# Performance work log

Measured on AMD Instinct MI355X. Metric: run time of the kernel, lower is better.

Reference implementation:

```python
import jax, jax.numpy as jnp
import numpy as np

E = 128          # embedding_dim
H = 128          # decoder_hidden_dim
N = 200000       # number of candidate nodes


def setup_inputs() -> dict:
    key = jax.random.key(0)
    k0, k1, k2, k3, k4, k5 = jax.random.split(key, 6)
    return {
        "current_node_emb": jax.random.normal(k0, (1, E), jnp.float32),
        "context_emb": jax.random.normal(k1, (1, E), jnp.float32),
        "candidate_node_embs": jax.random.normal(k2, (N, E), jnp.float32),
        "Wq": jax.random.normal(k3, (H, 2 * E), jnp.float32) * 0.05,  # nn.Linear(2E->H, bias=False) weight
        "Wk": jax.random.normal(k4, (H, E), jnp.float32) * 0.05,      # nn.Linear(E->H, bias=False) weight
        "mask": jax.random.randint(k5, (1, N), 0, 2, jnp.int32),
    }


def reference(current_node_emb, context_emb, candidate_node_embs, Wq, Wk, mask):
    # combined_input = cat([current, context], dim=1) -> [1, 2E]
    combined = jnp.concatenate([current_node_emb, context_emb], axis=1)
    query = combined @ Wq.T                      # [1, H]
    keys = candidate_node_embs @ Wk.T            # [N, H]
    attn_scores = query @ keys.T                 # [1, N]
    masked = jnp.where(mask == 0, -jnp.inf, attn_scores)
    probs = jax.nn.softmax(masked, axis=1)       # [1, N]

    n = probs.shape[1]
    k = min(50, max(1, int(0.5 * n)))            # static Python int -> jit-friendly
    top_probs, _ = jax.lax.top_k(probs, k)       # [1, k]
    threshold = top_probs[:, -1:]                # [1, 1]
    top_mask = probs >= threshold
    filtered = probs * top_mask
    filtered = filtered / (jnp.sum(filtered, axis=1, keepdims=True) + 1e-10)

    log_probs_all = jnp.log(filtered + 1e-10)    # [1, N]
    # Categorical(filtered): true-zero probability outside top-k
    logits = jnp.where(filtered > 0, jnp.log(filtered), -jnp.inf)
    action_idx = jax.random.categorical(jax.random.key(42), logits, axis=1)  # [1]
    log_prob_action = jnp.take_along_axis(logits, action_idx[:, None], axis=1)[:, 0]  # [1]
    return (log_probs_all, log_prob_action, action_idx)
```

## Files before the change

### kernel.cpp

```cpp
#include <hip/hip_runtime.h>
#include <math.h>


#define CAP 4096
#define NEG_INF (-__builtin_inff())

__device__ __forceinline__ unsigned int f2ord(float f){
  unsigned int b = __float_as_uint(f);
  return (b & 0x80000000u) ? ~b : (b | 0x80000000u);
}
__device__ __forceinline__ unsigned int rotl32(unsigned int x, int d){
  return (x << d) | (x >> (32 - d));
}

__device__ float gumbel_from_idx(unsigned int idx){
  unsigned int x0 = 0u, x1 = idx;
  const unsigned int ks0 = 0u, ks1 = 42u;
  const unsigned int ks2 = 0u ^ 42u ^ 0x1BD11BDAu;
  x0 += ks0; x1 += ks1;
#define TF_RND(r) { x0 += x1; x1 = rotl32(x1, (r)); x1 ^= x0; }
  TF_RND(13) TF_RND(15) TF_RND(26) TF_RND(6)
  x0 += ks1; x1 += ks2 + 1u;
  TF_RND(17) TF_RND(29) TF_RND(16) TF_RND(24)
  x0 += ks2; x1 += ks0 + 2u;
  TF_RND(13) TF_RND(15) TF_RND(26) TF_RND(6)
  x0 += ks0; x1 += ks1 + 3u;
  TF_RND(17) TF_RND(29) TF_RND(16) TF_RND(24)
  x0 += ks1; x1 += ks2 + 4u;
  TF_RND(13) TF_RND(15) TF_RND(26) TF_RND(6)
  x0 += ks2; x1 += ks0 + 5u;
#undef TF_RND
  unsigned int bits = x0 ^ x1;
  unsigned int fb = (bits >> 9) | 0x3f800000u;
  float f = __uint_as_float(fb) - 1.0f;
  float u = (f < 1.17549435e-38f) ? 1.17549435e-38f : f;
  return -logf(-logf(u));
}

__global__ void k_prep(const float* __restrict__ cur, const float* __restrict__ ctx,
                       const float* __restrict__ Wq, const float* __restrict__ Wk,
                       float* __restrict__ v, unsigned int* __restrict__ hist,
                       unsigned int* __restrict__ scal_u){
  __shared__ float comb[256];
  __shared__ float q[128];
  int t = threadIdx.x;
  for (int k = t; k < 2048; k += 256) hist[k] = 0u;
  if (t < 16) scal_u[t] = 0u;
  comb[t] = (t < 128) ? cur[t] : ctx[t - 128];
  __syncthreads();
  if (t < 128){
    float acc = 0.f;
    const float* row = Wq + t * 256;
    for (int j = 0; j < 256; ++j) acc = fmaf(row[j], comb[j], acc);
    q[t] = acc;
  }
  __syncthreads();
  if (t < 128){
    float acc = 0.f;
    for (int h = 0; h < 128; ++h) acc = fmaf(q[h], Wk[h * 128 + t], acc);
    v[t] = acc;
  }
}

__global__ __launch_bounds__(256) void k_score(const float* __restrict__ cand,
    const int* __restrict__ mask, const float* __restrict__ v,
    float* __restrict__ scores, float* __restrict__ out, int N){
  const float NLOG = logf(1e-10f);
  int t = threadIdx.x;
  int lane = t & 63, wave = t >> 6;
  int hi = lane >> 5, hl = lane & 31;
  float4 v4 = ((const float4*)v)[hl];
  const float4* cp = (const float4*)cand;
  int base = (blockIdx.x * 4 + wave) * 32;
  float4 c[16];
  #pragma unroll
  for (int k = 0; k < 16; ++k){
    int r = base + 2 * k + hi;
    r = (r < N) ? r : (N - 1);
    c[k] = cp[(size_t)r * 32 + hl];
  }
  float p[16];
  #pragma unroll
  for (int k = 0; k < 16; ++k)
    p[k] = fmaf(c[k].x, v4.x, fmaf(c[k].y, v4.y, fmaf(c[k].z, v4.z, c[k].w * v4.w)));
  #pragma unroll
  for (int k = 0; k < 16; ++k){
    p[k] += __shfl_xor(p[k], 1, 64);
    p[k] += __shfl_xor(p[k], 2, 64);
    p[k] += __shfl_xor(p[k], 4, 64);
    p[k] += __shfl_xor(p[k], 8, 64);
    p[k] += __shfl_xor(p[k], 16, 64);
  }
  float sv = p[0];
  #pragma unroll
  for (int k = 1; k < 16; ++k) sv = (hl == k) ? p[k] : sv;
  if (hl < 16){
    int r = base + 2 * hl + hi;
    if (r < N) scores[r] = mask[r] ? sv : NEG_INF;
  }
  int rr = blockIdx.x * 128 + t;
  if (t < 128 && rr < N) out[rr] = NLOG;
}

__global__ __launch_bounds__(256) void k_hist(const float* __restrict__ scores,
    unsigned int* __restrict__ hist, unsigned int* __restrict__ scal_u,
    int N, int ktop){
  __shared__ unsigned int lhist[2048];
  __shared__ float wsum[4];
  __shared__ int is_last;
  int t = threadIdx.x;
  int lane = t & 63, wave = t >> 6;
  for (int k = t; k < 2048; k += 256) lhist[k] = 0u;
  __syncthreads();
  float ez = 0.f;
  int i0 = (blockIdx.x * 256 + t) * 4;
  if (i0 + 3 < N){
    float4 s4 = *(const float4*)(scores + i0);
    float ss[4] = {s4.x, s4.y, s4.z, s4.w};
    #pragma unroll
    for (int e = 0; e < 4; ++e){
      if (ss[e] > NEG_INF){
        atomicAdd(&lhist[f2ord(ss[e]) >> 21], 1u);
        ez += expf(ss[e]);
      }
    }
  } else {
    for (int e = 0; e < 4; ++e){
      int i = i0 + e;
      if (i < N){
        float s = scores[i];
        if (s > NEG_INF){ atomicAdd(&lhist[f2ord(s) >> 21], 1u); ez += expf(s); }
      }
    }
  }
  #pragma unroll
  for (int off = 32; off; off >>= 1) ez += __shfl_xor(ez, off, 64);
  if (lane == 0) wsum[wave] = ez;
  __syncthreads();
  for (int k = t; k < 2048; k += 256){
    unsigned int c = lhist[k];
    if (c) atomicAdd(&hist[k], c);
  }
  if (t == 0) atomicAdd((float*)scal_u + 3, wsum[0] + wsum[1] + wsum[2] + wsum[3]);
  __syncthreads();
  if (t == 0){
    __threadfence();
    unsigned int old = atomicAdd(&scal_u[6], 1u);
    is_last = (old == gridDim.x - 1u);
  }
  __syncthreads();
  if (!is_last) return;
  __threadfence();
  __shared__ unsigned int suf[256];
  __shared__ int csel_sh;
  unsigned int csum = 0;
  for (int k = 0; k < 8; ++k) csum += hist[t * 8 + k];
  suf[t] = csum;
  if (t == 0) csel_sh = -1;
  __syncthreads();
  for (int d = 1; d < 256; d <<= 1){
    unsigned int add = (t + d < 256) ? suf[t + d] : 0u;
    __syncthreads();
    suf[t] += add;
    __syncthreads();
  }
  unsigned int st = suf[t];
  unsigned int sn = (t < 255) ? suf[t + 1] : 0u;
  if (st >= (unsigned)ktop && sn < (unsigned)ktop) csel_sh = t;
  __syncthreads();
  if (t == 0){
    int b_sel = 0;
    if (csel_sh >= 0){
      int c = csel_sh;
      unsigned int cum = (c < 255) ? suf[c + 1] : 0u;
      for (int b = 8 * c + 7; b >= 8 * c; --b){
        cum += hist[b];
        if (cum >= (unsigned)ktop){ b_sel = b; break; }
      }
    }
    scal_u[1] = ((unsigned int)b_sel) << 21;
  }
}

__global__ __launch_bounds__(256) void k_gather(const float* __restrict__ scores,
    unsigned int* __restrict__ scal_u, unsigned int* __restrict__ buf_idx,
    float* __restrict__ buf_s, float* __restrict__ out, int N, int ktop){
  int t = threadIdx.x;
  unsigned int u_lo = scal_u[1];
  int i0 = (blockIdx.x * 256 + t) * 4;
  if (i0 + 3 < N){
    float4 s4 = *(const float4*)(scores + i0);
    float ss[4] = {s4.x, s4.y, s4.z, s4.w};
    #pragma unroll
    for (int e = 0; e < 4; ++e){
      float s = ss[e];
      if (s > NEG_INF && f2ord(s) >= u_lo){
        unsigned int pos = atomicAdd(&scal_u[0], 1u);
        if (pos < CAP){ buf_idx[pos] = (unsigned int)(i0 + e); buf_s[pos] = s; }
      }
    }
  } else {
    for (int e = 0; e < 4; ++e){
      int i = i0 + e;
      if (i < N){
        float s = scores[i];
        if (s > NEG_INF && f2ord(s) >= u_lo){
          unsigned int pos = atomicAdd(&scal_u[0], 1u);
          if (pos < CAP){ buf_idx[pos] = (unsigned int)i; buf_s[pos] = s; }
        }
      }
    }
  }
  __syncthreads();
  __shared__ int is_last;
  if (t == 0){
    __threadfence();
    unsigned int old = atomicAdd(&scal_u[7], 1u);
    is_last = (old == gridDim.x - 1u);
  }
  __syncthreads();
  if (!is_last) return;
  __threadfence();
  float* scal_f = (float*)scal_u;
  __shared__ float s_lds[CAP];
  __shared__ float thr_sh;
  __shared__ float wred[4];
  __shared__ float rv[4], rl[4];
  __shared__ unsigned int ri[4];
  int C = (int)scal_u[0]; if (C > CAP) C = CAP;
  for (int j = t; j < C; j += 256) s_lds[j] = buf_s[j];
  if (t == 0) thr_sh = NEG_INF;
  __syncthreads();
  if (C > ktop){
    for (int j = t; j < C; j += 256){
      float sj = s_lds[j];
      int g = 0, e = 0;
      for (int k2 = 0; k2 < C; ++k2){
        float sk = s_lds[k2];
        g += (sk > sj);
        e += (sk == sj);
      }
      if (g < ktop && g + e >= ktop) thr_sh = sj;
    }
  }
  __syncthreads();
  float s_thr = thr_sh;
  float Z = scal_f[3];
  float part = 0.f;
  for (int j = t; j < C; j += 256){
    float sj = s_lds[j];
    if (sj >= s_thr) part += expf(sj);
  }
  #pragma unroll
  for (int off = 32; off; off >>= 1) part += __shfl_xor(part, off, 64);
  int wave = t >> 6, lane = t & 63;
  if (lane == 0) wred[wave] = part;
  __syncthreads();
  float T = wred[0] + wred[1] + wred[2] + wred[3];
  float D = T + 1e-10f * Z;
  float lnD = logf(D);
  for (int j = t; j < C; j += 256){
    float sj = s_lds[j];
    if (sj >= s_thr) out[buf_idx[j]] = logf(expf(sj - lnD) + 1e-10f);
  }
  float bestv = NEG_INF, bestlogit = NEG_INF;
  unsigned int bestidx = 0xFFFFFFFFu;
  for (int j = t; j < C; j += 256){
    float sj = s_lds[j];
    if (sj >= s_thr){
      unsigned int idx = buf_idx[j];
      float logit = sj - lnD;
      float val = logit + gumbel_from_idx(idx);
      if (val > bestv || (val == bestv && idx < bestidx)){
        bestv = val; bestlogit = logit; bestidx = idx;
      }
    }
  }
  #pragma unroll
  for (int off = 32; off; off >>= 1){
    float ov = __shfl_xor(bestv, off, 64);
    float ol = __shfl_xor(bestlogit, off, 64);
    unsigned int oi = (unsigned int)__shfl_xor((int)bestidx, off, 64);
    if (ov > bestv || (ov == bestv && oi < bestidx)){
      bestv = ov; bestlogit = ol; bestidx = oi;
    }
  }
  if (lane == 0){ rv[wave] = bestv; rl[wave] = bestlogit; ri[wave] = bestidx; }
  __syncthreads();
  if (t == 0){
    for (int w = 1; w < 4; ++w){
      if (rv[w] > rv[0] || (rv[w] == rv[0] && ri[w] < ri[0])){
        rv[0] = rv[w]; rl[0] = rl[w]; ri[0] = ri[w];
      }
    }
    out[N] = rl[0];
    out[N + 1] = (float)ri[0];
  }
}

extern "C" void kernel_launch(void* const* d_in, const int* in_sizes, int n_in,
                              void* d_out, int out_size, void* d_ws, size_t ws_size,
                              hipStream_t stream){
  const float* cur  = (const float*)d_in[0];
  const float* ctx  = (const float*)d_in[1];
  const float* cand = (const float*)d_in[2];
  const float* Wq   = (const float*)d_in[3];
  const float* Wk   = (const float*)d_in[4];
  const int*   mask = (const int*)d_in[5];
  int N = in_sizes[5];
  float* out = (float*)d_out;

  char* ws = (char*)d_ws;
  unsigned int* scal_u  = (unsigned int*)ws;
  unsigned int* hist    = (unsigned int*)(ws + 256);
  float*        v       = (float*)(ws + 256 + 8192);
  float*        scores  = (float*)(ws + 256 + 8192 + 512);
  char*         bufbase = ws + 256 + 8192 + 512 + 800000;
  unsigned int* buf_idx = (unsigned int*)bufbase;
  float*        buf_s   = (float*)(bufbase + CAP * 4);

  int ktop = N / 2; if (ktop < 1) ktop = 1; if (ktop > 50) ktop = 50;

  int g_score = (N + 127) / 128;
  int g_pass  = (N + 1023) / 1024;

  k_prep<<<1, 256, 0, stream>>>(cur, ctx, Wq, Wk, v, hist, scal_u);
  k_score<<<g_score, 256, 0, stream>>>(cand, mask, v, scores, out, N);
  k_hist<<<g_pass, 256, 0, stream>>>(scores, hist, scal_u, N, ktop);
  k_gather<<<g_pass, 256, 0, stream>>>(scores, scal_u, buf_idx, buf_s, out, N, ktop);
}
```

Baseline: 208.2 us.

## Fuse histogram and exp-sum into score kernel, recompute threshold per gather block

Moves the radix histogram and softmax-denominator accumulation into the scoring kernel, which removes the separate k_hist pass that re-read all scores. Global histogram atomics are spread across eight copies, as are the partial sums of Z, to reduce contention. Each k_gather block now reduces the eight copies and finds the top-k bucket itself, replacing the last-block election. In exchange every gather block repeats a 16K-entry histogram read and prefix scan, and the score kernel takes on LDS atomics plus 2048 global atomics per block.

```diff
diff --git a/kernel.cpp b/kernel.cpp
--- a/kernel.cpp
+++ b/kernel.cpp
@@ -4,6 +4,7 @@
 
 #define CAP 4096
 #define NEG_INF (-__builtin_inff())
+#define NHC 8
 
 __device__ __forceinline__ unsigned int f2ord(float f){
   unsigned int b = __float_as_uint(f);
@@ -39,12 +40,12 @@
 
 __global__ void k_prep(const float* __restrict__ cur, const float* __restrict__ ctx,
                        const float* __restrict__ Wq, const float* __restrict__ Wk,
-                       float* __restrict__ v, unsigned int* __restrict__ hist,
+                       float* __restrict__ v, unsigned int* __restrict__ ghist,
                        unsigned int* __restrict__ scal_u){
   __shared__ float comb[256];
   __shared__ float q[128];
   int t = threadIdx.x;
-  for (int k = t; k < 2048; k += 256) hist[k] = 0u;
+  for (int k = t; k < NHC * 2048; k += 256) ghist[k] = 0u;
   if (t < 16) scal_u[t] = 0u;
   comb[t] = (t < 128) ? cur[t] : ctx[t - 128];
   __syncthreads();
@@ -64,11 +65,16 @@
 
 __global__ __launch_bounds__(256) void k_score(const float* __restrict__ cand,
     const int* __restrict__ mask, const float* __restrict__ v,
-    float* __restrict__ scores, float* __restrict__ out, int N){
+    float* __restrict__ scores, float* __restrict__ out,
+    unsigned int* __restrict__ ghist, unsigned int* __restrict__ scal_u, int N){
+  __shared__ unsigned int lhist[2048];
+  __shared__ float wsum[4];
   const float NLOG = logf(1e-10f);
   int t = threadIdx.x;
   int lane = t & 63, wave = t >> 6;
   int hi = lane >> 5, hl = lane & 31;
+  for (int k = t; k < 2048; k += 256) lhist[k] = 0u;
+  __syncthreads();
   float4 v4 = ((const float4*)v)[hl];
   const float4* cp = (const float4*)cand;
   int base = (blockIdx.x * 4 + wave) * 32;
@@ -94,69 +100,55 @@
   float sv = p[0];
   #pragma unroll
   for (int k = 1; k < 16; ++k) sv = (hl == k) ? p[k] : sv;
+  float ez = 0.f;
   if (hl < 16){
     int r = base + 2 * hl + hi;
-    if (r < N) scores[r] = mask[r] ? sv : NEG_INF;
+    if (r < N){
+      int m = mask[r];
+      float s = m ? sv : NEG_INF;
+      scores[r] = s;
+      if (m){
+        atomicAdd(&lhist[f2ord(s) >> 21], 1u);
+        ez = expf(s);
+      }
+    }
   }
   int rr = blockIdx.x * 128 + t;
   if (t < 128 && rr < N) out[rr] = NLOG;
-}
-
-__global__ __launch_bounds__(256) void k_hist(const float* __restrict__ scores,
-    unsigned int* __restrict__ hist, unsigned int* __restrict__ scal_u,
-    int N, int ktop){
-  __shared__ unsigned int lhist[2048];
-  __shared__ float wsum[4];
-  __shared__ int is_last;
-  int t = threadIdx.x;
-  int lane = t & 63, wave = t >> 6;
-  for (int k = t; k < 2048; k += 256) lhist[k] = 0u;
-  __syncthreads();
-  float ez = 0.f;
-  int i0 = (blockIdx.x * 256 + t) * 4;
-  if (i0 + 3 < N){
-    float4 s4 = *(const float4*)(scores + i0);
-    float ss[4] = {s4.x, s4.y, s4.z, s4.w};
-    #pragma unroll
-    for (int e = 0; e < 4; ++e){
-      if (ss[e] > NEG_INF){
-        atomicAdd(&lhist[f2ord(ss[e]) >> 21], 1u);
-        ez += expf(ss[e]);
-      }
-    }
-  } else {
-    for (int e = 0; e < 4; ++e){
-      int i = i0 + e;
-      if (i < N){
-        float s = scores[i];
-        if (s > NEG_INF){ atomicAdd(&lhist[f2ord(s) >> 21], 1u); ez += expf(s); }
-      }
-    }
-  }
   #pragma unroll
   for (int off = 32; off; off >>= 1) ez += __shfl_xor(ez, off, 64);
   if (lane == 0) wsum[wave] = ez;
   __syncthreads();
+  unsigned int hbase = (blockIdx.x & (NHC - 1)) * 2048u;
   for (int k = t; k < 2048; k += 256){
-    unsigned int c = lhist[k];
-    if (c) atomicAdd(&hist[k], c);
-  }
-  if (t == 0) atomicAdd((float*)scal_u + 3, wsum[0] + wsum[1] + wsum[2] + wsum[3]);
-  __syncthreads();
-  if (t == 0){
-    __threadfence();
-    unsigned int old = atomicAdd(&scal_u[6], 1u);
-    is_last = (old == gridDim.x - 1u);
-  }
-  __syncthreads();
-  if (!is_last) return;
-  __threadfence();
+    unsigned int cc = lhist[k];
+    if (cc) atomicAdd(&ghist[hbase + k], cc);
+  }
+  if (t == 0)
+    atomicAdd((float*)scal_u + 8 + (blockIdx.x & (NHC - 1)),
+              wsum[0] + wsum[1] + wsum[2] + wsum[3]);
+}
+
+__global__ __launch_bounds__(256) void k_gather(const float* __restrict__ scores,
+    const unsigned int* __restrict__ ghist, unsigned int* __restrict__ scal_u,
+    unsigned int* __restrict__ buf_idx, float* __restrict__ buf_s,
+    float* __restrict__ out, int N, int ktop){
+  __shared__ unsigned int hsum[2048];
   __shared__ unsigned int suf[256];
   __shared__ int csel_sh;
+  __shared__ unsigned int ulo_sh;
+  int t = threadIdx.x;
+  for (int k = t; k < 2048; k += 256){
+    unsigned int s = 0;
+    #pragma unroll
+    for (int c = 0; c < NHC; ++c) s += ghist[c * 2048 + k];
+    hsum[k] = s;
+  }
+  if (t == 0) csel_sh = -1;
+  __syncthreads();
   unsigned int csum = 0;
-  for (int k = 0; k < 8; ++k) csum += hist[t * 8 + k];
+  for (int k = 0; k < 8; ++k) csum += hsum[t * 8 + k];
   suf[t] = csum;
-  if (t == 0) csel_sh = -1;
   __syncthreads();
   for (int d = 1; d < 256; d <<= 1){
     unsigned int add = (t + d < 256) ? suf[t + d] : 0u;
@@ -174,19 +166,14 @@
       int c = csel_sh;
       unsigned int cum = (c < 255) ? suf[c + 1] : 0u;
       for (int b = 8 * c + 7; b >= 8 * c; --b){
-        cum += hist[b];
+        cum += hsum[b];
         if (cum >= (unsigned)ktop){ b_sel = b; break; }
       }
     }
-    scal_u[1] = ((unsigned int)b_sel) << 21;
-  }
-}
-
-__global__ __launch_bounds__(256) void k_gather(const float* __restrict__ scores,
-    unsigned int* __restrict__ scal_u, unsigned int* __restrict__ buf_idx,
-    float* __restrict__ buf_s, float* __restrict__ out, int N, int ktop){
-  int t = threadIdx.x;
-  unsigned int u_lo = scal_u[1];
+    ulo_sh = ((unsigned int)b_sel) << 21;
+  }
+  __syncthreads();
+  unsigned int u_lo = ulo_sh;
   int i0 = (blockIdx.x * 256 + t) * 4;
   if (i0 + 3 < N){
     float4 s4 = *(const float4*)(scores + i0);
@@ -245,7 +232,9 @@
   }
   __syncthreads();
   float s_thr = thr_sh;
-  float Z = scal_f[3];
+  float Z = 0.f;
+  #pragma unroll
+  for (int c = 0; c < NHC; ++c) Z += scal_f[8 + c];
   float part = 0.f;
   for (int j = t; j < C; j += 256){
     float sj = s_lds[j];
@@ -312,10 +301,10 @@
 
   char* ws = (char*)d_ws;
   unsigned int* scal_u  = (unsigned int*)ws;
-  unsigned int* hist    = (unsigned int*)(ws + 256);
-  float*        v       = (float*)(ws + 256 + 8192);
-  float*        scores  = (float*)(ws + 256 + 8192 + 512);
-  char*         bufbase = ws + 256 + 8192 + 512 + 800000;
+  unsigned int* ghist   = (unsigned int*)(ws + 256);
+  float*        v       = (float*)(ws + 256 + 65536);
+  float*        scores  = (float*)(ws + 256 + 65536 + 512);
+  char*         bufbase = ws + 256 + 65536 + 512 + 800000;
   unsigned int* buf_idx = (unsigned int*)bufbase;
   float*        buf_s   = (float*)(bufbase + CAP * 4);
 
@@ -324,8 +313,7 @@
   int g_score = (N + 127) / 128;
   int g_pass  = (N + 1023) / 1024;
 
-  k_prep<<<1, 256, 0, stream>>>(cur, ctx, Wq, Wk, v, hist, scal_u);
-  k_score<<<g_score, 256, 0, stream>>>(cand, mask, v, scores, out, N);
-  k_hist<<<g_pass, 256, 0, stream>>>(scores, hist, scal_u, N, ktop);
-  k_gather<<<g_pass, 256, 0, stream>>>(scores, scal_u, buf_idx, buf_s, out, N, ktop);
-}
+  k_prep<<<1, 256, 0, stream>>>(cur, ctx, Wq, Wk, v, ghist, scal_u);
+  k_score<<<g_score, 256, 0, stream>>>(cand, mask, v, scores, out, ghist, scal_u, N);
+  k_gather<<<g_pass, 256, 0, stream>>>(scores, ghist, scal_u, buf_idx, buf_s, out, N, ktop);
+}
```

Result: no change. 210.9 us (+1.3%).
